# Performance work log

Hardware: AMD Instinct MI355X
Metric: run time of the kernel (lower is better)

The kernel has to match this reference:

```python
import jax, jax.numpy as jnp
import numpy as np
import math

L = 2          # num_layers
H = 1024       # hidden_dim
NH = 16        # num_heads
HD = H // NH   # head_dim = 64
M = 4096       # mlp_dim
GRIDS = [(2, 32, 32), (1, 32, 32)]  # (t,h,w) per image -> 2048 + 1024 = 3072 tokens
THETA = 10000.0
EPS = 1e-5


def _rope_cos_sin(grids, head_dim):
    # Rope2DPosEmbRepeated: interleaved (x,y) complex rotations, repeated over t.
    n = head_dim // 4
    freqs = 1.0 / (THETA ** (np.arange(0, head_dim, 4, dtype=np.float64)[:n] / head_dim))
    parts = []
    for t, h, w in grids:
        ys, xs = np.meshgrid(np.arange(h), np.arange(w), indexing='ij')
        xa = xs.reshape(-1, 1).astype(np.float64) * freqs  # [h*w, n]
        ya = ys.reshape(-1, 1).astype(np.float64) * freqs
        ang = np.stack([xa, ya], axis=-1).reshape(-1, head_dim // 2)  # interleave x,y
        parts.append(np.tile(ang, (t, 1)))
    ang = np.concatenate(parts, axis=0).astype(np.float32)  # [S, head_dim//2]
    return jnp.asarray(np.cos(ang)), jnp.asarray(np.sin(ang))


def _segment_ids(grids):
    lens = [t * h * w for t, h, w in grids]
    return jnp.asarray(np.repeat(np.arange(len(lens)), lens))


def _layernorm(x, g, b):
    mu = jnp.mean(x, axis=-1, keepdims=True)
    var = jnp.mean(jnp.square(x - mu), axis=-1, keepdims=True)
    return (x - mu) * jax.lax.rsqrt(var + EPS) * g + b


def _apply_rope(x, cos, sin):
    # x: [S, NH, HD]; cos/sin: [S, HD//2] -> broadcast over heads (unsqueeze(-2))
    xr = x.reshape(x.shape[0], x.shape[1], HD // 2, 2)
    a, b = xr[..., 0], xr[..., 1]
    c = cos[:, None, :]
    s = sin[:, None, :]
    oa = a * c - b * s
    ob = a * s + b * c
    return jnp.stack([oa, ob], axis=-1).reshape(x.shape)


def setup_inputs() -> dict:
    key = jax.random.key(0)
    ks = jax.random.split(key, 8)
    S = sum(t * h * w for t, h, w in GRIDS)
    sH = 1.0 / math.sqrt(H)
    sM = 1.0 / math.sqrt(M)
    return {
        'hidden_states': jax.random.normal(ks[0], (S, H), jnp.float32),
        'grid_thws': jnp.asarray(np.array(GRIDS, dtype=np.int32)),
        'ln0_g': jnp.ones((L, H), jnp.float32),
        'ln0_b': jnp.zeros((L, H), jnp.float32),
        'wqkv': jax.random.normal(ks[1], (L, 3 * H, H), jnp.float32) * sH,
        'wo': jax.random.normal(ks[2], (L, H, H), jnp.float32) * sH,
        'ln1_g': jnp.ones((L, H), jnp.float32),
        'ln1_b': jnp.zeros((L, H), jnp.float32),
        'fc0_w': jax.random.normal(ks[3], (L, M, H), jnp.float32) * math.sqrt(2.0 / H),
        'fc0_b': jnp.zeros((L, M), jnp.float32),
        'fc1_w': jax.random.normal(ks[4], (L, H, M), jnp.float32) * math.sqrt(2.0 / M),
        'fc1_b': jnp.zeros((L, H), jnp.float32),
        'fln_g': jnp.ones((H,), jnp.float32),
        'fln_b': jnp.zeros((H,), jnp.float32),
    }


def reference(hidden_states, grid_thws, ln0_g, ln0_b, wqkv, wo, ln1_g, ln1_b,
              fc0_w, fc0_b, fc1_w, fc1_b, fln_g, fln_b):
    grids = [tuple(int(v) for v in row) for row in np.asarray(grid_thws)]
    S = hidden_states.shape[0]
    cos, sin = _rope_cos_sin(grids, HD)
    seg = _segment_ids(grids)
    mask = seg[:, None] == seg[None, :]  # block-diagonal [S, S]
    scale = 1.0 / math.sqrt(HD)

    x = hidden_states
    for i in range(L):
        h = _layernorm(x, ln0_g[i], ln0_b[i])
        qkv = (h @ wqkv[i].T).reshape(S, 3, NH, HD)
        q, k, v = qkv[:, 0], qkv[:, 1], qkv[:, 2]
        q = _apply_rope(q, cos, sin)
        k = _apply_rope(k, cos, sin)
        scores = jnp.einsum('qhd,khd->hqk', q, k) * scale
        scores = jnp.where(mask[None], scores, -1e30)
        attn = jax.nn.softmax(scores, axis=-1)
        o = jnp.einsum('hqk,khd->qhd', attn, v).reshape(S, H)
        x = x + o @ wo[i].T
        h2 = _layernorm(x, ln1_g[i], ln1_b[i])
        mlp = jax.nn.gelu(h2 @ fc0_w[i].T + fc0_b[i], approximate=False) @ fc1_w[i].T + fc1_b[i]
        x = x + mlp
    return _layernorm(x, fln_g, fln_b)
```

## Files before the change

kernel.cpp:

```cpp
#include <hip/hip_runtime.h>
#include <hip/hip_bf16.h>
#include <cstdint>
#include <math.h>

constexpr int ST   = 3072;
constexpr int HH   = 1024;
constexpr int NHD  = 16;
constexpr int DH   = 64;
constexpr int MMLP = 4096;
constexpr int SEG0 = 2048;

using short8 = __attribute__((ext_vector_type(8))) short;
using f32x4  = __attribute__((ext_vector_type(4))) float;

#if __has_builtin(__builtin_amdgcn_exp2f)
#define EXP2F __builtin_amdgcn_exp2f
#else
#define EXP2F exp2f
#endif

__device__ __forceinline__ unsigned short f2bf(float f) {
  unsigned int u = __float_as_uint(f);
  u += 0x7fffu + ((u >> 16) & 1u);
  return (unsigned short)(u >> 16);
}

__device__ __forceinline__ void g2l16(const void* g, void* l) {
  __builtin_amdgcn_global_load_lds(
      (const __attribute__((address_space(1))) unsigned int*)g,
      (__attribute__((address_space(3))) unsigned int*)l, 16, 0, 0);
}

__global__ void f32_to_bf16(const float* __restrict__ src,
                            unsigned short* __restrict__ dst, int n4) {
  const int i = blockIdx.x * blockDim.x + threadIdx.x;
  if (i >= n4) return;
  const float4 v = ((const float4*)src)[i];
  ushort4 u;
  u.x = f2bf(v.x); u.y = f2bf(v.y); u.z = f2bf(v.z); u.w = f2bf(v.w);
  ((ushort4*)dst)[i] = u;
}

__global__ void ln_kernel(const float* __restrict__ x,
                          const float* __restrict__ g,
                          const float* __restrict__ b,
                          unsigned short* obf) {
  const int s = blockIdx.x;
  const int t = threadIdx.x;
  const float4 v = ((const float4*)(x + (size_t)s * HH))[t];
  float s1 = v.x + v.y + v.z + v.w;
  float s2 = v.x * v.x + v.y * v.y + v.z * v.z + v.w * v.w;
#pragma unroll
  for (int off = 32; off > 0; off >>= 1) {
    s1 += __shfl_down(s1, off);
    s2 += __shfl_down(s2, off);
  }
  __shared__ float red[8];
  __shared__ float stat[2];
  const int wv = t >> 6, ln = t & 63;
  if (ln == 0) { red[wv] = s1; red[4 + wv] = s2; }
  __syncthreads();
  if (t == 0) {
    float a1 = red[0] + red[1] + red[2] + red[3];
    float a2 = red[4] + red[5] + red[6] + red[7];
    float mu = a1 * (1.f / HH);
    float var = a2 * (1.f / HH) - mu * mu;
    stat[0] = mu;
    stat[1] = rsqrtf(var + 1e-5f);
  }
  __syncthreads();
  const float mu = stat[0], rs = stat[1];
  const float4 gg = ((const float4*)g)[t];
  const float4 bb = ((const float4*)b)[t];
  ushort4 u;
  u.x = f2bf((v.x - mu) * rs * gg.x + bb.x);
  u.y = f2bf((v.y - mu) * rs * gg.y + bb.y);
  u.z = f2bf((v.z - mu) * rs * gg.z + bb.z);
  u.w = f2bf((v.w - mu) * rs * gg.w + bb.w);
  ((ushort4*)(obf + (size_t)s * HH))[t] = u;
}

__global__ void ln_comb(const float* __restrict__ xin,
                        const float* __restrict__ P,
                        const float* __restrict__ bias,
                        const float* __restrict__ g,
                        const float* __restrict__ b,
                        float* __restrict__ xout,
                        unsigned short* obf, float* of) {
  const int s = blockIdx.x;
  const int t = threadIdx.x;
  const size_t row = (size_t)s * HH;
  const size_t sl = (size_t)ST * HH;
  float4 v = ((const float4*)(xin + row))[t];
  const float4 p0 = ((const float4*)(P + row))[t];
  const float4 p1 = ((const float4*)(P + sl + row))[t];
  const float4 p2 = ((const float4*)(P + 2 * sl + row))[t];
  const float4 p3 = ((const float4*)(P + 3 * sl + row))[t];
  v.x += p0.x + p1.x + p2.x + p3.x;
  v.y += p0.y + p1.y + p2.y + p3.y;
  v.z += p0.z + p1.z + p2.z + p3.z;
  v.w += p0.w + p1.w + p2.w + p3.w;
  if (bias) {
    const float4 bb4 = ((const float4*)bias)[t];
    v.x += bb4.x; v.y += bb4.y; v.z += bb4.z; v.w += bb4.w;
  }
  if (xout) ((float4*)(xout + row))[t] = v;
  float s1 = v.x + v.y + v.z + v.w;
  float s2 = v.x * v.x + v.y * v.y + v.z * v.z + v.w * v.w;
#pragma unroll
  for (int off = 32; off > 0; off >>= 1) {
    s1 += __shfl_down(s1, off);
    s2 += __shfl_down(s2, off);
  }
  __shared__ float red[8];
  __shared__ float stat[2];
  const int wv = t >> 6, ln = t & 63;
  if (ln == 0) { red[wv] = s1; red[4 + wv] = s2; }
  __syncthreads();
  if (t == 0) {
    float a1 = red[0] + red[1] + red[2] + red[3];
    float a2 = red[4] + red[5] + red[6] + red[7];
    float mu = a1 * (1.f / HH);
    float var = a2 * (1.f / HH) - mu * mu;
    stat[0] = mu;
    stat[1] = rsqrtf(var + 1e-5f);
  }
  __syncthreads();
  const float mu = stat[0], rs = stat[1];
  const float4 gg = ((const float4*)g)[t];
  const float4 bb = ((const float4*)b)[t];
  float4 o;
  o.x = (v.x - mu) * rs * gg.x + bb.x;
  o.y = (v.y - mu) * rs * gg.y + bb.y;
  o.z = (v.z - mu) * rs * gg.z + bb.z;
  o.w = (v.w - mu) * rs * gg.w + bb.w;
  if (obf) {
    ushort4 u;
    u.x = f2bf(o.x); u.y = f2bf(o.y); u.z = f2bf(o.z); u.w = f2bf(o.w);
    ((ushort4*)(obf + row))[t] = u;
  } else {
    ((float4*)(of + row))[t] = o;
  }
}

__global__ void rope_tables(float* __restrict__ cosb, float* __restrict__ sinb) {
  const int s = blockIdx.x;
  const int j = threadIdx.x;
  const int p = (s < SEG0) ? (s & 1023) : (s - SEG0);
  const int pos = (j & 1) ? (p >> 5) : (p & 31);
  const int f = j >> 1;
  const double freq = pow(10000.0, -(double)f / 16.0);
  const double ang = (double)pos * freq;
  cosb[s * 32 + j] = (float)cos(ang);
  sinb[s * 32 + j] = (float)sin(ang);
}

__global__ void rope_kernel(const float* __restrict__ qkv,
                            const float* __restrict__ cosb,
                            const float* __restrict__ sinb,
                            unsigned short* __restrict__ Qb,
                            unsigned short* __restrict__ Kb,
                            unsigned short* __restrict__ Vb) {
  const int s = blockIdx.x;
  const int t = threadIdx.x;
  const size_t base = (size_t)s * 3072;
  const size_t obase = (size_t)s * HH;
  const float SQ = 0.125f * 1.4426950408889634f;
#pragma unroll
  for (int p = t; p < 512; p += 256) {
    const int jp = p & 31;
    const float c = cosb[s * 32 + jp];
    const float sn = sinb[s * 32 + jp];
    const int off = (p >> 5) * 64 + jp * 2;
    float a = qkv[base + off], b = qkv[base + off + 1];
    unsigned int w = f2bf((a * c - b * sn) * SQ) |
                     ((unsigned int)f2bf((a * sn + b * c) * SQ) << 16);
    *(unsigned int*)(Qb + obase + off) = w;
    a = qkv[base + 1024 + off]; b = qkv[base + 1024 + off + 1];
    w = f2bf(a * c - b * sn) | ((unsigned int)f2bf(a * sn + b * c) << 16);
    *(unsigned int*)(Kb + obase + off) = w;
    a = qkv[base + 2048 + off]; b = qkv[base + 2048 + off + 1];
    w = f2bf(a) | ((unsigned int)f2bf(b) << 16);
    *(unsigned int*)(Vb + obase + off) = w;
  }
}

__global__ void v_transpose(const unsigned short* __restrict__ Vb,
                            unsigned short* __restrict__ VT) {
  const int h = blockIdx.y;
  const int s0 = blockIdx.x * 64;
  const int tid = threadIdx.x;
  __shared__ unsigned short T[64][72];
  const int tr = tid >> 3, pc = tid & 7;
#pragma unroll
  for (int it = 0; it < 2; ++it) {
    short8 v = *(const short8*)(Vb + (size_t)(s0 + it * 32 + tr) * HH + h * DH + pc * 8);
    *(short8*)&T[it * 32 + tr][pc * 8] = v;
  }
  __syncthreads();
  const int d = tid >> 2;
  const int c0 = (tid & 3) * 16;
  short8 o0, o1;
#pragma unroll
  for (int j = 0; j < 8; ++j) { o0[j] = T[c0 + j][d]; o1[j] = T[c0 + 8 + j][d]; }
  unsigned short* dst = VT + (size_t)(h * 64 + d) * ST + s0 + c0;
  *(short8*)dst = o0;
  *(short8*)(dst + 8) = o1;
}

template <int MODE>
__launch_bounds__(256)
__global__ void gemm_bt(const unsigned short* __restrict__ A,
                        const unsigned short* __restrict__ B,
                        float* Cf, unsigned short* Cb,
                        const float* __restrict__ bias,
                        int N, int K) {
  __shared__ unsigned short Al[128 * 64];
  __shared__ unsigned short Bl[128 * 64];
  const int tid = threadIdx.x;
  const int lane = tid & 63;
  const int wave = tid >> 6;
  const int col = lane & 15;
  const int quad = lane >> 4;
  const int m0 = blockIdx.y * 128;
  const int n0 = blockIdx.x * 128;
  const int wm = (wave & 1) * 64;
  const int wn = (wave >> 1) * 64;

  int kFrom = 0, kTo = K;
  if (MODE == 4) {
    const int kc = K / gridDim.z;
    kFrom = blockIdx.z * kc;
    kTo = kFrom + kc;
  }

  f32x4 acc[4][4] = {};

  const int tr = tid >> 3;
  const int pb = tid & 7;
  const int kb = pb ^ (tr & 7);
  const unsigned short* Ag = A + (size_t)(m0 + tr) * K + kb * 8;
  const unsigned short* Bg = B + (size_t)(n0 + tr) * K + kb * 8;
  unsigned short* Alw = Al + (size_t)tid * 8;
  unsigned short* Blw = Bl + (size_t)tid * 8;

  for (int k0 = kFrom; k0 < kTo; k0 += 64) {
#pragma unroll
    for (int it = 0; it < 4; ++it) {
      g2l16(Ag + (size_t)(it * 32) * K + k0, Alw + it * 2048);
      g2l16(Bg + (size_t)(it * 32) * K + k0, Blw + it * 2048);
    }
    __syncthreads();
#pragma unroll
    for (int kk = 0; kk < 2; ++kk) {
      short8 af[4], bfr[4];
#pragma unroll
      for (int mt = 0; mt < 4; ++mt) {
        int r = wm + mt * 16 + col;
        int kp = (kk * 4 + quad) ^ (r & 7);
        af[mt] = *(const short8*)(Al + r * 64 + kp * 8);
      }
#pragma unroll
      for (int nt = 0; nt < 4; ++nt) {
        int r = wn + nt * 16 + col;
        int kp = (kk * 4 + quad) ^ (r & 7);
        bfr[nt] = *(const short8*)(Bl + r * 64 + kp * 8);
      }
#pragma unroll
      for (int mt = 0; mt < 4; ++mt)
#pragma unroll
        for (int nt = 0; nt < 4; ++nt)
          acc[mt][nt] = __builtin_amdgcn_mfma_f32_16x16x32_bf16(
              af[mt], bfr[nt], acc[mt][nt], 0, 0, 0);
    }
    __syncthreads();
  }
  const size_t zoff = (MODE == 4) ? (size_t)blockIdx.z * ST * N : 0;
#pragma unroll
  for (int mt = 0; mt < 4; ++mt) {
#pragma unroll
    for (int r = 0; r < 4; ++r) {
      const int gr = m0 + wm + mt * 16 + quad * 4 + r;
#pragma unroll
      for (int nt = 0; nt < 4; ++nt) {
        const int gc = n0 + wn + nt * 16 + col;
        const float v = acc[mt][nt][r];
        const size_t idx = (size_t)gr * N + gc;
        if (MODE == 0) {
          Cf[idx] = v;
        } else if (MODE == 2) {
          const float tt = v + bias[gc];
          const float gl = 0.5f * tt * (1.f + erff(tt * 0.70710678118654752f));
          Cb[idx] = f2bf(gl);
        } else {
          Cf[zoff + idx] = v;
        }
      }
    }
  }
}

__launch_bounds__(256)
__global__ void attn_flash(const unsigned short* __restrict__ Qb,
                           const unsigned short* __restrict__ Kb,
                           const unsigned short* __restrict__ VT,
                           float* __restrict__ Op01,
                           float* __restrict__ Op23,
                           float* __restrict__ lbuf) {
  const int h = blockIdx.y;
  const int unit = blockIdx.x;
  int qt, chunk, s0;
  if (unit < 64) { qt = unit >> 2; chunk = unit & 3; s0 = 0; }
  else { const int v = unit - 64; qt = 16 + (v >> 1); chunk = v & 1; s0 = SEG0; }
  const int q0 = qt * 128;
  const int koff = s0 + chunk * 512;

  const int tid = threadIdx.x;
  const int lane = tid & 63;
  const int wave = tid >> 6;
  const int col = lane & 15;
  const int quad = lane >> 4;

  __shared__ unsigned short Kl[128 * 64];
  __shared__ unsigned short Vl[64 * 128];
  __shared__ unsigned int Pl[4][2][2][16][20];

  short8 qf[2][2];
#pragma unroll
  for (int mt = 0; mt < 2; ++mt) {
    const unsigned short* qrow =
        Qb + (size_t)(q0 + wave * 32 + mt * 16 + col) * HH + h * DH;
    qf[mt][0] = *(const short8*)(qrow + quad * 8);
    qf[mt][1] = *(const short8*)(qrow + 32 + quad * 8);
  }

  short8 ones;
#pragma unroll
  for (int j = 0; j < 8; ++j) ones[j] = (short)0x3F80;

  f32x4 accO[2][4] = {};
  f32x4 accL[2] = {};
  const float SHIFT = 16.f;

  const int trK = tid >> 3, pbK = tid & 7;
  const int kbK = pbK ^ (trK & 7);
  const int trV = tid >> 4, pbV = tid & 15;

  for (int kb0 = 0; kb0 < 512; kb0 += 128) {
#pragma unroll
    for (int it = 0; it < 4; ++it)
      g2l16(Kb + (size_t)(koff + kb0 + it * 32 + trK) * HH + h * DH + kbK * 8,
            (unsigned short*)Kl + it * 2048 + (size_t)tid * 8);
#pragma unroll
    for (int it = 0; it < 4; ++it) {
      const int d = it * 16 + trV;
      const int kbv = pbV ^ (d & 7);
      g2l16(VT + (size_t)(h * 64 + d) * ST + koff + kb0 + kbv * 8,
            (unsigned short*)Vl + it * 2048 + (size_t)tid * 8);
    }
    __syncthreads();

    f32x4 sc[2][8];
#pragma unroll
    for (int nt = 0; nt < 8; ++nt) {
      const int r = nt * 16 + col;
      const short8 kf0 = *(const short8*)(Kl + r * 64 + ((quad) ^ (r & 7)) * 8);
      const short8 kf1 = *(const short8*)(Kl + r * 64 + ((4 + quad) ^ (r & 7)) * 8);
#pragma unroll
      for (int mt = 0; mt < 2; ++mt) {
        f32x4 z = {};
        z = __builtin_amdgcn_mfma_f32_16x16x32_bf16(kf0, qf[mt][0], z, 0, 0, 0);
        sc[mt][nt] = __builtin_amdgcn_mfma_f32_16x16x32_bf16(kf1, qf[mt][1], z, 0, 0, 0);
      }
    }

#pragma unroll
    for (int kd = 0; kd < 4; ++kd) {
      const int par = kd & 1;
#pragma unroll
      for (int mt = 0; mt < 2; ++mt) {
#pragma unroll
        for (int ntl = 0; ntl < 2; ++ntl) {
          const f32x4 s4 = sc[mt][kd * 2 + ntl];
          const float p0 = EXP2F(s4[0] - SHIFT);
          const float p1 = EXP2F(s4[1] - SHIFT);
          const float p2 = EXP2F(s4[2] - SHIFT);
          const float p3 = EXP2F(s4[3] - SHIFT);
          uint2 w;
          w.x = (unsigned)f2bf(p0) | ((unsigned)f2bf(p1) << 16);
          w.y = (unsigned)f2bf(p2) | ((unsigned)f2bf(p3) << 16);
          *(uint2*)&Pl[wave][par][mt][col][ntl * 8 + quad * 2] = w;
        }
      }
      short8 pf[2];
#pragma unroll
      for (int mt = 0; mt < 2; ++mt)
        pf[mt] = *(const short8*)&Pl[wave][par][mt][col][quad * 4];
#pragma unroll
      for (int mt = 0; mt < 2; ++mt)
        accL[mt] = __builtin_amdgcn_mfma_f32_16x16x32_bf16(pf[mt], ones,
                                                           accL[mt], 0, 0, 0);
#pragma unroll
      for (int dt = 0; dt < 4; ++dt) {
        const int rv = dt * 16 + col;
        const int pbv2 = (kd * 4 + quad) ^ (rv & 7);
        const short8 vf = *(const short8*)(Vl + rv * 128 + pbv2 * 8);
#pragma unroll
        for (int mt = 0; mt < 2; ++mt)
          accO[mt][dt] = __builtin_amdgcn_mfma_f32_16x16x32_bf16(
              pf[mt], vf, accO[mt][dt], 0, 0, 0);
      }
    }
    __syncthreads();
  }

  float* Op = (chunk < 2) ? (Op01 + (size_t)chunk * (ST * HH))
                          : (Op23 + (size_t)(chunk - 2) * (ST * HH));
#pragma unroll
  for (int mt = 0; mt < 2; ++mt)
#pragma unroll
    for (int r = 0; r < 4; ++r) {
      const int row = q0 + wave * 32 + mt * 16 + quad * 4 + r;
#pragma unroll
      for (int dt = 0; dt < 4; ++dt)
        Op[(size_t)row * HH + h * DH + dt * 16 + col] = accO[mt][dt][r];
      if (col == 0)
        lbuf[((size_t)chunk * ST + row) * NHD + h] = accL[mt][r];
    }
}

__global__ void attn_combine(const float* __restrict__ Op01,
                             const float* __restrict__ Op23,
                             const float* __restrict__ lbuf,
                             unsigned short* __restrict__ out) {
  const int s = blockIdx.x;
  const int t = threadIdx.x;
  const int h = t >> 4;
  const int d0 = (t & 15) * 4;
  const int nc = (s < SEG0) ? 4 : 2;
  float L = 0.f;
  float4 o = make_float4(0.f, 0.f, 0.f, 0.f);
  for (int c = 0; c < nc; ++c) {
    L += lbuf[((size_t)c * ST + s) * NHD + h];
    const float* Op = (c < 2) ? (Op01 + (size_t)c * (ST * HH))
                              : (Op23 + (size_t)(c - 2) * (ST * HH));
    const float4 v = *(const float4*)(Op + (size_t)s * HH + h * DH + d0);
    o.x += v.x; o.y += v.y; o.z += v.z; o.w += v.w;
  }
  const float inv = 1.f / L;
  ushort4 u;
  u.x = f2bf(o.x * inv); u.y = f2bf(o.y * inv);
  u.z = f2bf(o.z * inv); u.w = f2bf(o.w * inv);
  ((ushort4*)(out + (size_t)s * HH))[t] = u;
}

extern "C" void kernel_launch(void* const* d_in, const int* in_sizes, int n_in,
                              void* d_out, int out_size, void* d_ws, size_t ws_size,
                              hipStream_t stream) {
  const float* hs   = (const float*)d_in[0];
  const float* ln0g = (const float*)d_in[2];
  const float* ln0b = (const float*)d_in[3];
  const float* wqkv = (const float*)d_in[4];
  const float* wo   = (const float*)d_in[5];
  const float* ln1g = (const float*)d_in[6];
  const float* ln1b = (const float*)d_in[7];
  const float* fc0w = (const float*)d_in[8];
  const float* fc0b = (const float*)d_in[9];
  const float* fc1w = (const float*)d_in[10];
  const float* fc1b = (const float*)d_in[11];
  const float* flng = (const float*)d_in[12];
  const float* flnb = (const float*)d_in[13];

  char* ws = (char*)d_ws;
  unsigned short* wqkv_bf = (unsigned short*)(ws + 0);
  unsigned short* wo_bf   = (unsigned short*)(ws + 12582912);
  unsigned short* fc0_bf  = (unsigned short*)(ws + 16777216);
  unsigned short* fc1_bf  = (unsigned short*)(ws + 33554432);
  float*          x       = (float*)(ws + 50331648);
  unsigned short* abf     = (unsigned short*)(ws + 62914560);
  unsigned short* gelu_bf = (unsigned short*)(ws + 69206016);
  float*          qkvC    = (float*)(ws + 94371840);
  unsigned short* Qbf     = (unsigned short*)(ws + 132120576);
  unsigned short* Kbf     = (unsigned short*)(ws + 138412032);
  unsigned short* Vbf     = (unsigned short*)(ws + 144703488);
  float*          cosb    = (float*)(ws + 150994944);
  float*          sinb    = (float*)(ws + 151388160);
  unsigned short* VT    = (unsigned short*)(ws + 94371840);
  float*          Op01  = (float*)(ws + 100663296);
  float*          Op23  = (float*)(ws + 69206016);
  float*          lbuf  = (float*)(ws + 144703488);
  float*          Pbuf  = (float*)(ws + 94371840);

  f32_to_bf16<<<6144, 256, 0, stream>>>(wqkv, wqkv_bf, 1572864);
  f32_to_bf16<<<2048, 256, 0, stream>>>(wo, wo_bf, 524288);
  f32_to_bf16<<<8192, 256, 0, stream>>>(fc0w, fc0_bf, 2097152);
  f32_to_bf16<<<8192, 256, 0, stream>>>(fc1w, fc1_bf, 2097152);
  rope_tables<<<ST, 32, 0, stream>>>(cosb, sinb);

  for (int i = 0; i < 2; ++i) {
    if (i == 0)
      ln_kernel<<<ST, 256, 0, stream>>>(hs, ln0g, ln0b, abf);
    gemm_bt<0><<<dim3(24, 24), 256, 0, stream>>>(
        abf, wqkv_bf + (size_t)i * 3 * HH * HH, qkvC, nullptr, nullptr,
        3 * HH, HH);
    rope_kernel<<<ST, 256, 0, stream>>>(qkvC, cosb, sinb, Qbf, Kbf, Vbf);
    v_transpose<<<dim3(48, 16), 256, 0, stream>>>(Vbf, VT);
    attn_flash<<<dim3(80, 16), 256, 0, stream>>>(Qbf, Kbf, VT, Op01, Op23, lbuf);
    attn_combine<<<ST, 256, 0, stream>>>(Op01, Op23, lbuf, abf);
    gemm_bt<4><<<dim3(8, 24, 4), 256, 0, stream>>>(
        abf, wo_bf + (size_t)i * HH * HH, Pbuf, nullptr, nullptr, HH, HH);
    ln_comb<<<ST, 256, 0, stream>>>(
        (i == 0) ? hs : x, Pbuf, nullptr, ln1g + i * HH, ln1b + i * HH,
        x, abf, nullptr);
    gemm_bt<2><<<dim3(32, 24), 256, 0, stream>>>(
        abf, fc0_bf + (size_t)i * MMLP * HH, nullptr, gelu_bf, fc0b + i * MMLP,
        MMLP, HH);
    gemm_bt<4><<<dim3(8, 24, 4), 256, 0, stream>>>(
        gelu_bf, fc1_bf + (size_t)i * HH * MMLP, Pbuf, nullptr, nullptr,
        HH, MMLP);
    if (i == 0)
      ln_comb<<<ST, 256, 0, stream>>>(x, Pbuf, fc1b, ln0g + HH, ln0b + HH,
                                      x, abf, nullptr);
    else
      ln_comb<<<ST, 256, 0, stream>>>(x, Pbuf, fc1b + HH, flng, flnb,
                                      nullptr, nullptr, (float*)d_out);
  }
}
```

Baseline: 659.6 us.

## Fuse RoPE into QKV GEMM epilogue, fast erf GELU, halve split-K

The QKV GEMM now applies RoPE, the Q scale and the bf16 conversion in its epilogue, using a lane shuffle to fetch each rotation pair partner. It writes Q, K and V directly, which removes the fp32 qkv buffer and the separate rope kernel. GELU now uses an Abramowitz-Stegun erf approximation built on hardware rcp and exp2 in place of erff. The split-K factor for the Wo and fc1 GEMMs drops from 4 to 2, which halves the partial-sum traffic that ln_comb must read. In exchange, the approximate erf adds a small numerical error, and the smaller split gives the grid fewer blocks to run in parallel.

```diff
diff --git a/kernel.cpp b/kernel.cpp
--- a/kernel.cpp
+++ b/kernel.cpp
@@ -19,6 +19,12 @@
 #define EXP2F exp2f
 #endif
 
+#if __has_builtin(__builtin_amdgcn_rcpf)
+#define RCPF __builtin_amdgcn_rcpf
+#else
+#define RCPF(x) (1.f / (x))
+#endif
+
 __device__ __forceinline__ unsigned short f2bf(float f) {
   unsigned int u = __float_as_uint(f);
   u += 0x7fffu + ((u >> 16) & 1u);
@@ -29,6 +35,19 @@
   __builtin_amdgcn_global_load_lds(
       (const __attribute__((address_space(1))) unsigned int*)g,
       (__attribute__((address_space(3))) unsigned int*)l, 16, 0, 0);
+}
+
+__device__ __forceinline__ float erf_fast(float z) {
+  const float az = fabsf(z);
+  const float t1 = RCPF(1.f + 0.3275911f * az);
+  const float poly =
+      t1 * (0.254829592f +
+            t1 * (-0.284496736f +
+                  t1 * (1.421413741f +
+                        t1 * (-1.453152027f + t1 * 1.061405429f))));
+  const float e = EXP2F(-az * az * 1.4426950408889634f);
+  const float v = 1.f - poly * e;
+  return (z < 0.f) ? -v : v;
 }
 
 __global__ void f32_to_bf16(const float* __restrict__ src,
@@ -80,6 +99,7 @@
   ((ushort4*)(obf + (size_t)s * HH))[t] = u;
 }
 
+template <int NS>
 __global__ void ln_comb(const float* __restrict__ xin,
                         const float* __restrict__ P,
                         const float* __restrict__ bias,
@@ -92,14 +112,11 @@
   const size_t row = (size_t)s * HH;
   const size_t sl = (size_t)ST * HH;
   float4 v = ((const float4*)(xin + row))[t];
-  const float4 p0 = ((const float4*)(P + row))[t];
-  const float4 p1 = ((const float4*)(P + sl + row))[t];
-  const float4 p2 = ((const float4*)(P + 2 * sl + row))[t];
-  const float4 p3 = ((const float4*)(P + 3 * sl + row))[t];
-  v.x += p0.x + p1.x + p2.x + p3.x;
-  v.y += p0.y + p1.y + p2.y + p3.y;
-  v.z += p0.z + p1.z + p2.z + p3.z;
-  v.w += p0.w + p1.w + p2.w + p3.w;
+#pragma unroll
+  for (int c = 0; c < NS; ++c) {
+    const float4 p = ((const float4*)(P + c * sl + row))[t];
+    v.x += p.x; v.y += p.y; v.z += p.z; v.w += p.w;
+  }
   if (bias) {
     const float4 bb4 = ((const float4*)bias)[t];
     v.x += bb4.x; v.y += bb4.y; v.z += bb4.z; v.w += bb4.w;
@@ -155,36 +172,6 @@
   sinb[s * 32 + j] = (float)sin(ang);
 }
 
-__global__ void rope_kernel(const float* __restrict__ qkv,
-                            const float* __restrict__ cosb,
-                            const float* __restrict__ sinb,
-                            unsigned short* __restrict__ Qb,
-                            unsigned short* __restrict__ Kb,
-                            unsigned short* __restrict__ Vb) {
-  const int s = blockIdx.x;
-  const int t = threadIdx.x;
-  const size_t base = (size_t)s * 3072;
-  const size_t obase = (size_t)s * HH;
-  const float SQ = 0.125f * 1.4426950408889634f;
-#pragma unroll
-  for (int p = t; p < 512; p += 256) {
-    const int jp = p & 31;
-    const float c = cosb[s * 32 + jp];
-    const float sn = sinb[s * 32 + jp];
-    const int off = (p >> 5) * 64 + jp * 2;
-    float a = qkv[base + off], b = qkv[base + off + 1];
-    unsigned int w = f2bf((a * c - b * sn) * SQ) |
-                     ((unsigned int)f2bf((a * sn + b * c) * SQ) << 16);
-    *(unsigned int*)(Qb + obase + off) = w;
-    a = qkv[base + 1024 + off]; b = qkv[base + 1024 + off + 1];
-    w = f2bf(a * c - b * sn) | ((unsigned int)f2bf(a * sn + b * c) << 16);
-    *(unsigned int*)(Kb + obase + off) = w;
-    a = qkv[base + 2048 + off]; b = qkv[base + 2048 + off + 1];
-    w = f2bf(a) | ((unsigned int)f2bf(b) << 16);
-    *(unsigned int*)(Vb + obase + off) = w;
-  }
-}
-
 __global__ void v_transpose(const unsigned short* __restrict__ Vb,
                             unsigned short* __restrict__ VT) {
   const int h = blockIdx.y;
@@ -214,6 +201,7 @@
                         const unsigned short* __restrict__ B,
                         float* Cf, unsigned short* Cb,
                         const float* __restrict__ bias,
+                        const float* __restrict__ bias2,
                         int N, int K) {
   __shared__ unsigned short Al[128 * 64];
   __shared__ unsigned short Bl[128 * 64];
@@ -276,6 +264,8 @@
     __syncthreads();
   }
   const size_t zoff = (MODE == 4) ? (size_t)blockIdx.z * ST * N : 0;
+  const int bufsel = (MODE == 5) ? (n0 >> 10) : 0;
+  const float SQ = 0.125f * 1.4426950408889634f;
 #pragma unroll
   for (int mt = 0; mt < 4; ++mt) {
 #pragma unroll
@@ -285,15 +275,26 @@
       for (int nt = 0; nt < 4; ++nt) {
         const int gc = n0 + wn + nt * 16 + col;
         const float v = acc[mt][nt][r];
-        const size_t idx = (size_t)gr * N + gc;
-        if (MODE == 0) {
-          Cf[idx] = v;
-        } else if (MODE == 2) {
+        if (MODE == 2) {
           const float tt = v + bias[gc];
-          const float gl = 0.5f * tt * (1.f + erff(tt * 0.70710678118654752f));
-          Cb[idx] = f2bf(gl);
+          const float gl = 0.5f * tt * (1.f + erf_fast(tt * 0.70710678f));
+          Cb[(size_t)gr * N + gc] = f2bf(gl);
+        } else if (MODE == 4) {
+          Cf[zoff + (size_t)gr * N + gc] = v;
         } else {
-          Cf[zoff + idx] = v;
+          const int c1023 = gc & 1023;
+          unsigned short* out = Cb + (size_t)bufsel * (ST * HH);
+          if (bufsel == 2) {
+            out[(size_t)gr * HH + c1023] = f2bf(v);
+          } else {
+            const int j = (c1023 & 63) >> 1;
+            const float cs = bias[gr * 32 + j];
+            const float sn = bias2[gr * 32 + j];
+            const float vp = __shfl_xor(v, 1);
+            float res = (lane & 1) ? (vp * sn + v * cs) : (v * cs - vp * sn);
+            if (bufsel == 0) res *= SQ;
+            out[(size_t)gr * HH + c1023] = f2bf(res);
+          }
         }
       }
     }
@@ -479,7 +480,6 @@
   float*          x       = (float*)(ws + 50331648);
   unsigned short* abf     = (unsigned short*)(ws + 62914560);
   unsigned short* gelu_bf = (unsigned short*)(ws + 69206016);
-  float*          qkvC    = (float*)(ws + 94371840);
   unsigned short* Qbf     = (unsigned short*)(ws + 132120576);
   unsigned short* Kbf     = (unsigned short*)(ws + 138412032);
   unsigned short* Vbf     = (unsigned short*)(ws + 144703488);
@@ -500,29 +500,29 @@
   for (int i = 0; i < 2; ++i) {
     if (i == 0)
       ln_kernel<<<ST, 256, 0, stream>>>(hs, ln0g, ln0b, abf);
-    gemm_bt<0><<<dim3(24, 24), 256, 0, stream>>>(
-        abf, wqkv_bf + (size_t)i * 3 * HH * HH, qkvC, nullptr, nullptr,
+    gemm_bt<5><<<dim3(24, 24), 256, 0, stream>>>(
+        abf, wqkv_bf + (size_t)i * 3 * HH * HH, nullptr, Qbf, cosb, sinb,
         3 * HH, HH);
-    rope_kernel<<<ST, 256, 0, stream>>>(qkvC, cosb, sinb, Qbf, Kbf, Vbf);
     v_transpose<<<dim3(48, 16), 256, 0, stream>>>(Vbf, VT);
     attn_flash<<<dim3(80, 16), 256, 0, stream>>>(Qbf, Kbf, VT, Op01, Op23, lbuf);
     attn_combine<<<ST, 256, 0, stream>>>(Op01, Op23, lbuf, abf);
-    gemm_bt<4><<<dim3(8, 24, 4), 256, 0, stream>>>(
-        abf, wo_bf + (size_t)i * HH * HH, Pbuf, nullptr, nullptr, HH, HH);
-    ln_comb<<<ST, 256, 0, stream>>>(
+    gemm_bt<4><<<dim3(8, 24, 2), 256, 0, stream>>>(
+        abf, wo_bf + (size_t)i * HH * HH, Pbuf, nullptr, nullptr, nullptr,
+        HH, HH);
+    ln_comb<2><<<ST, 256, 0, stream>>>(
         (i == 0) ? hs : x, Pbuf, nullptr, ln1g + i * HH, ln1b + i * HH,
         x, abf, nullptr);
     gemm_bt<2><<<dim3(32, 24), 256, 0, stream>>>(
         abf, fc0_bf + (size_t)i * MMLP * HH, nullptr, gelu_bf, fc0b + i * MMLP,
-        MMLP, HH);
-    gemm_bt<4><<<dim3(8, 24, 4), 256, 0, stream>>>(
+        nullptr, MMLP, HH);
+    gemm_bt<4><<<dim3(8, 24, 2), 256, 0, stream>>>(
         gelu_bf, fc1_bf + (size_t)i * HH * MMLP, Pbuf, nullptr, nullptr,
-        HH, MMLP);
+        nullptr, HH, MMLP);
     if (i == 0)
-      ln_comb<<<ST, 256, 0, stream>>>(x, Pbuf, fc1b, ln0g + HH, ln0b + HH,
-                                      x, abf, nullptr);
+      ln_comb<2><<<ST, 256, 0, stream>>>(x, Pbuf, fc1b, ln0g + HH, ln0b + HH,
+                                         x, abf, nullptr);
     else
-      ln_comb<<<ST, 256, 0, stream>>>(x, Pbuf, fc1b + HH, flng, flnb,
-                                      nullptr, nullptr, (float*)d_out);
-  }
-}
+      ln_comb<2><<<ST, 256, 0, stream>>>(x, Pbuf, fc1b + HH, flng, flnb,
+                                         nullptr, nullptr, (float*)d_out);
+  }
+}
```

Result: faster. 640.9 us (-2.8%).
